# Optimization experiments

Measured on AMD Instinct MI355X. Metric: run time of the kernel, lower is better.

The kernel has to match this reference:

```python
import jax, jax.numpy as jnp
import numpy as np
from jax.ops import segment_sum, segment_max

N_NODES = 100000
N_EDGES = 1600000
F_DIM = 64
N_GRAPHS = 64
K_HOPS = 3
EPS = 1e-5


def setup_inputs() -> dict:
    key = jax.random.key(0)
    ks = jax.random.split(key, 8)
    x = jax.random.normal(ks[0], (N_NODES, F_DIM), dtype=jnp.float32)
    edge_index = jax.random.randint(ks[1], (2, N_EDGES), 0, N_NODES, dtype=jnp.int32)
    batch = jnp.sort(jax.random.randint(ks[2], (N_NODES,), 0, N_GRAPHS, dtype=jnp.int32))
    edge_weight = jax.random.uniform(ks[3], (N_EDGES,), dtype=jnp.float32)
    # TAGConv params: K+1 hop-wise linear weights (no per-lin bias) + one output bias
    W = jax.random.normal(ks[4], (K_HOPS + 1, F_DIM, F_DIM), dtype=jnp.float32) * 0.05
    b = jnp.zeros((F_DIM,), dtype=jnp.float32)
    # GraphNorm params
    gn_weight = jnp.ones((F_DIM,), dtype=jnp.float32)
    gn_bias = jnp.zeros((F_DIM,), dtype=jnp.float32)
    gn_mean_scale = jnp.ones((F_DIM,), dtype=jnp.float32)
    return {"x": x, "edge_index": edge_index, "batch": batch, "edge_weight": edge_weight,
            "W": W, "b": b, "gn_weight": gn_weight, "gn_bias": gn_bias,
            "gn_mean_scale": gn_mean_scale}


def reference(x, edge_index, batch, edge_weight, W, b, gn_weight, gn_bias, gn_mean_scale):
    src, dst = edge_index[0], edge_index[1]

    # --- TAGConv: gcn_norm without self-loops ---
    deg = segment_sum(edge_weight, dst, num_segments=N_NODES)            # [N]
    dis = jnp.where(deg > 0, jax.lax.rsqrt(deg), 0.0)                    # deg^{-1/2}, inf -> 0
    norm = dis[src] * edge_weight * dis[dst]                             # [E]

    # out = sum_k (A_norm^k x) W_k + b
    out = x @ W[0]
    h = x
    for k in range(1, K_HOPS + 1):
        h = segment_sum(norm[:, None] * h[src], dst, num_segments=N_NODES)  # [N, F]
        out = out + h @ W[k]
    out = out + b

    # --- GraphNorm: per-graph mean/var with learnable mean_scale ---
    cnt = segment_sum(jnp.ones((N_NODES,), out.dtype), batch, num_segments=N_GRAPHS)
    cnt = jnp.maximum(cnt, 1.0)[:, None]                                  # [G, 1]
    mean = segment_sum(out, batch, num_segments=N_GRAPHS) / cnt          # [G, F]
    centered = out - mean[batch] * gn_mean_scale                         # [N, F]
    var = segment_sum(centered * centered, batch, num_segments=N_GRAPHS) / cnt
    hn = gn_weight * centered / jnp.sqrt(var + EPS)[batch] + gn_bias

    # --- residual + ReLU (add_residue=True) ---
    h_emb = jax.nn.relu(hn + x)                                          # [N, F]

    # --- global mean + max pooling ---
    mean_pool = segment_sum(h_emb, batch, num_segments=N_GRAPHS) / cnt   # [G, F]
    max_pool = segment_max(h_emb, batch, num_segments=N_GRAPHS)          # [G, F]
    flat = jnp.concatenate([mean_pool, max_pool], axis=-1)               # [G, 2F]

    return (h_emb, flat)
```

## Files before the change

kernel.cpp:

```cpp
#include <hip/hip_runtime.h>
#include <hip/hip_bf16.h>

#define NN 100000
#define NE 1600000
#define NG 64
#define FD 64
#define EPSV 1e-5f

typedef __hip_bfloat16 bf16;
typedef __attribute__((ext_vector_type(8))) short bf16x8;
typedef __attribute__((ext_vector_type(4))) float f32x4;

__device__ __forceinline__ float ldb(bf16 v) { return __bfloat162float(v); }
__device__ __forceinline__ bf16 f2b(float v) { return __float2bfloat16(v); }
__device__ __forceinline__ float b2f_bits(short s) {
    return __uint_as_float(((unsigned)(unsigned short)s) << 16);
}

#define NB1 391
#define CB 625
#define EPB 2560
#define CCN (NB1 * CB)
#define SCB2 ((CCN + 2047) / 2048)

__device__ __forceinline__ int xcd_chunk(int bid, int nwg) {
    int q = nwg >> 3, r = nwg & 7;
    int xcd = bid & 7, j = bid >> 3;
    return (xcd < r ? xcd * (q + 1) : r * (q + 1) + (xcd - r) * q) + j;
}

constexpr size_t ALGN(size_t x) { return (x + 255) & ~(size_t)255; }
constexpr size_t OFF_GSUM = 0;
constexpr size_t OFF_GSSQ = OFF_GSUM + ALGN((size_t)NG * FD * 4);
constexpr size_t OFF_GCNT = OFF_GSSQ + ALGN((size_t)NG * FD * 4);
constexpr size_t OFF_PSUM = OFF_GCNT + ALGN((size_t)NG * 4);
constexpr size_t OFF_PMAX = OFF_PSUM + ALGN((size_t)NG * FD * 4);
constexpr size_t ZERO_BYTES = OFF_PMAX + ALGN((size_t)NG * FD * 4);
constexpr size_t OFF_CNT  = ZERO_BYTES;
constexpr size_t OFF_DIS  = OFF_CNT  + ALGN((size_t)NN * 4);
constexpr size_t OFF_ROWP = OFF_DIS  + ALGN((size_t)NN * 4);
constexpr size_t OFF_BSUM = OFF_ROWP + ALGN((size_t)NN * 4);
constexpr size_t OFF_WT   = OFF_BSUM + ALGN(256 * 4);
constexpr size_t OFF_CSR  = OFF_WT   + ALGN(16384 * 2);
constexpr size_t OFF_H    = OFF_CSR  + ALGN((size_t)NE * 8);
constexpr size_t OFF_OUT  = OFF_H    + ALGN((size_t)NN * 256 * 2);
constexpr size_t OFF_CSRT = OFF_OUT;
constexpr size_t OFF_CC   = OFF_CSRT + ALGN((size_t)NE * 8);
static_assert(OFF_CC + (size_t)CCN * 4 - OFF_OUT <= (size_t)NN * FD * 4, "alias overflow");

#define XCB 6250
__global__ __launch_bounds__(256) void coarse_fused_kernel(const int* __restrict__ dst,
                                                           int* __restrict__ cc,
                                                           const float* __restrict__ x,
                                                           bf16* __restrict__ H,
                                                           const float* __restrict__ W,
                                                           bf16* __restrict__ Wt) {
    int b = blockIdx.x;
    if (b < CB) {
        __shared__ int hist[NB1];
        for (int i = threadIdx.x; i < NB1; i += 256) hist[i] = 0;
        __syncthreads();
        int e0 = b * EPB + threadIdx.x;
        #pragma unroll
        for (int i = 0; i < EPB / 256; i++)
            atomicAdd(&hist[dst[e0 + i * 256] >> 8], 1);
        __syncthreads();
        for (int i = threadIdx.x; i < NB1; i += 256)
            cc[(size_t)i * CB + b] = hist[i];
    } else if (b < CB + XCB) {
        int i = (b - CB) * 256 + threadIdx.x;
        float4 xv = ((const float4*)x)[i];
        bf16 t0 = f2b(xv.x), t1 = f2b(xv.y), t2 = f2b(xv.z), t3 = f2b(xv.w);
        ushort4 o;
        o.x = *(unsigned short*)&t0; o.y = *(unsigned short*)&t1;
        o.z = *(unsigned short*)&t2; o.w = *(unsigned short*)&t3;
        ((ushort4*)H)[i] = o;
    } else {
        int i = (b - CB - XCB) * 256 + threadIdx.x;
        int n = i & 63, kk = i >> 6;
        Wt[n * 256 + kk] = f2b(W[kk * 64 + n]);
    }
}

#define SCAN_BLK 256
#define SCAN_ITEMS 8
__global__ __launch_bounds__(SCAN_BLK) void scan_blocks(int* __restrict__ data,
                                                        int* __restrict__ bsum, int n) {
    __shared__ int lds[SCAN_BLK];
    int t = threadIdx.x, b = blockIdx.x;
    int base = b * SCAN_BLK * SCAN_ITEMS + t * SCAN_ITEMS;
    int v[SCAN_ITEMS];
    int s = 0;
    #pragma unroll
    for (int i = 0; i < SCAN_ITEMS; i++) {
        int idx = base + i;
        v[i] = (idx < n) ? data[idx] : 0;
        s += v[i];
    }
    lds[t] = s;
    __syncthreads();
    for (int off = 1; off < SCAN_BLK; off <<= 1) {
        int x = (t >= off) ? lds[t - off] : 0;
        __syncthreads();
        lds[t] += x;
        __syncthreads();
    }
    int excl = lds[t] - s;
    if (t == SCAN_BLK - 1) bsum[b] = lds[t];
    int run = excl;
    #pragma unroll
    for (int i = 0; i < SCAN_ITEMS; i++) {
        int idx = base + i;
        if (idx < n) data[idx] = run;
        run += v[i];
    }
}

__global__ __launch_bounds__(256) void scatter2_kernel(const int* __restrict__ src,
                                                       const int* __restrict__ dst,
                                                       const float* __restrict__ ew,
                                                       const int* __restrict__ cc,
                                                       const int* __restrict__ bsum,
                                                       int2* __restrict__ csrt) {
    __shared__ int sc[512];
    __shared__ int bp[128];
    __shared__ int gdel[NB1];
    __shared__ int2 stage[EPB];
    __shared__ int sdel[EPB];
    int t = threadIdx.x;
    int L = xcd_chunk(blockIdx.x, CB);

    sc[t] = 0; sc[t + 256] = 0;
    if (t < 128) bp[t] = (t < SCB2) ? bsum[t] : 0;
    __syncthreads();

    int br[EPB / 256], px[EPB / 256], pw[EPB / 256];
    #pragma unroll
    for (int i = 0; i < EPB / 256; i++) {
        int e = L * EPB + i * 256 + t;
        int d = dst[e];
        int bk = d >> 8;
        int rk = atomicAdd(&sc[bk], 1);
        br[i] = bk | (rk << 9);
        px[i] = src[e] | ((d & 255) << 17);
        pw[i] = __float_as_int(ew[e]);
    }
    __syncthreads();

    for (int off = 1; off < 512; off <<= 1) {
        int a0 = (t >= off) ? sc[t - off] : 0;
        int a1 = sc[t + 256 - off];
        int a2 = (off < 128 && t < 128 && t >= off) ? bp[t - off] : 0;
        __syncthreads();
        sc[t] += a0; sc[t + 256] += a1;
        if (off < 128 && t < 128) bp[t] += a2;
        __syncthreads();
    }

    for (int i = t; i < NB1; i += 256) {
        int idx = i * CB + L;
        int k = idx >> 11;
        int gpref = (k > 0) ? bp[k - 1] : 0;
        gdel[i] = cc[idx] + gpref - ((i > 0) ? sc[i - 1] : 0);
    }
    __syncthreads();

    #pragma unroll
    for (int i = 0; i < EPB / 256; i++) {
        int bk = br[i] & 511;
        int rk = br[i] >> 9;
        int slot = ((bk > 0) ? sc[bk - 1] : 0) + rk;
        stage[slot] = make_int2(px[i], pw[i]);
        sdel[slot] = gdel[bk];
    }
    __syncthreads();

    for (int j = t; j < EPB; j += 256)
        csrt[(size_t)(sdel[j] + j)] = stage[j];
}

__global__ __launch_bounds__(256) void fine_kernel(const int* __restrict__ cc,
                                                   const int* __restrict__ bsum,
                                                   const int2* __restrict__ csrt,
                                                   int2* __restrict__ csr,
                                                   int* __restrict__ rowp,
                                                   int* __restrict__ cnts,
                                                   float* __restrict__ dis) {
    __shared__ int hist[256];
    __shared__ float degw[256];
    __shared__ int pref[256];
    __shared__ int fcur[256];
    __shared__ int bp[128];
    __shared__ int bounds[2];
    int b = blockIdx.x;
    int t = threadIdx.x;
    hist[t] = 0; degw[t] = 0.f;
    if (t < 128) bp[t] = (t < SCB2) ? bsum[t] : 0;
    __syncthreads();
    for (int off = 1; off < 128; off <<= 1) {
        int x = (t < 128 && t >= off) ? bp[t - off] : 0;
        __syncthreads();
        if (t < 128) bp[t] += x;
        __syncthreads();
    }
    if (t == 0) {
        int i0 = b * CB, k0 = i0 >> 11;
        bounds[0] = cc[i0] + ((k0 > 0) ? bp[k0 - 1] : 0);
        if (b == NB1 - 1) bounds[1] = NE;
        else {
            int i1 = (b + 1) * CB, k1 = i1 >> 11;
            bounds[1] = cc[i1] + ((k1 > 0) ? bp[k1 - 1] : 0);
        }
    }
    __syncthreads();
    int base = bounds[0];
    int cnt = bounds[1] - base;

    for (int j = t; j < cnt; j += 256) {
        int2 e = csrt[base + j];
        int f = e.x >> 17;
        atomicAdd(&hist[f], 1);
        atomicAdd(&degw[f], __int_as_float(e.y));
    }
    __syncthreads();
    int hv = hist[t];
    pref[t] = hv;
    __syncthreads();
    for (int off = 1; off < 256; off <<= 1) {
        int x = (t >= off) ? pref[t - off] : 0;
        __syncthreads();
        pref[t] += x;
        __syncthreads();
    }
    int ex = pref[t] - hv;
    fcur[t] = ex;
    int node = b * 256 + t;
    if (node < NN) {
        rowp[node] = base + ex;
        cnts[node] = hv;
        float s = degw[t];
        dis[node] = (s > 0.f) ? rsqrtf(s) : 0.f;
    }
    __syncthreads();
    for (int j = t; j < cnt; j += 256) {
        int2 e = csrt[base + j];
        int f = e.x >> 17;
        int pos = atomicAdd(&fcur[f], 1);
        csr[base + pos] = make_int2(e.x & 0x1FFFF, e.y);
    }
}

template <bool FIRST>
__device__ __forceinline__ void row_accum_gen(const bf16* __restrict__ hin,
                                              int2* cp, int cnt,
                                              const float* __restrict__ dis,
                                              int sub, int fl, float a[8]) {
    if (cnt <= 24) {
        int2 e0 = (sub < cnt) ? cp[sub] : make_int2(0, 0);
        int2 e1 = (8 + sub < cnt) ? cp[8 + sub] : make_int2(0, 0);
        int2 e2 = (16 + sub < cnt) ? cp[16 + sub] : make_int2(0, 0);
        bf16x8 v0 = *(const bf16x8*)(hin + (size_t)e0.x * 64 + fl * 8);
        bf16x8 v1 = *(const bf16x8*)(hin + (size_t)e1.x * 64 + fl * 8);
        bf16x8 v2 = *(const bf16x8*)(hin + (size_t)e2.x * 64 + fl * 8);
        float w0 = __int_as_float(e0.y);
        float w1 = __int_as_float(e1.y);
        float w2 = __int_as_float(e2.y);
        if (FIRST) {
            w0 *= dis[e0.x]; w1 *= dis[e1.x]; w2 *= dis[e2.x];
            if (fl == 0) {
                if (sub < cnt)      cp[sub].y      = __float_as_int(w0);
                if (8 + sub < cnt)  cp[8 + sub].y  = __float_as_int(w1);
                if (16 + sub < cnt) cp[16 + sub].y = __float_as_int(w2);
            }
        }
        #pragma unroll
        for (int i = 0; i < 8; i++)
            a[i] += w0 * b2f_bits(v0[i]) + w1 * b2f_bits(v1[i]) + w2 * b2f_bits(v2[i]);
    } else {
        float b[8] = {0, 0, 0, 0, 0, 0, 0, 0};
        int j = 0;
        for (; j + 16 <= cnt; j += 16) {
            int2 e0 = cp[j + sub];
            int2 e1 = cp[j + 8 + sub];
            bf16x8 v0 = *(const bf16x8*)(hin + (size_t)e0.x * 64 + fl * 8);
            bf16x8 v1 = *(const bf16x8*)(hin + (size_t)e1.x * 64 + fl * 8);
            float w0 = __int_as_float(e0.y);
            float w1 = __int_as_float(e1.y);
            if (FIRST) {
                w0 *= dis[e0.x]; w1 *= dis[e1.x];
                if (fl == 0) {
                    cp[j + sub].y     = __float_as_int(w0);
                    cp[j + 8 + sub].y = __float_as_int(w1);
                }
            }
            #pragma unroll
            for (int i = 0; i < 8; i++) a[i] += w0 * b2f_bits(v0[i]);
            #pragma unroll
            for (int i = 0; i < 8; i++) b[i] += w1 * b2f_bits(v1[i]);
        }
        for (; j < cnt; j += 8) {
            int jj = j + sub;
            int2 e = (jj < cnt) ? cp[jj] : make_int2(0, 0);
            bf16x8 v = *(const bf16x8*)(hin + (size_t)e.x * 64 + fl * 8);
            float w = __int_as_float(e.y);
            if (FIRST) {
                w *= dis[e.x];
                if (fl == 0 && jj < cnt) cp[jj].y = __float_as_int(w);
            }
            #pragma unroll
            for (int i = 0; i < 8; i++) a[i] += w * b2f_bits(v[i]);
        }
        #pragma unroll
        for (int i = 0; i < 8; i++) a[i] += b[i];
    }
}

template <bool FIRST>
__global__ __launch_bounds__(256) void hop_kernel(const bf16* __restrict__ hin,
                                                  bf16* __restrict__ hout,
                                                  const int* __restrict__ rowp,
                                                  const int* __restrict__ cnts,
                                                  int2* __restrict__ csr,
                                                  const float* __restrict__ dis) {
    int pair = blockIdx.x * 4 + (threadIdx.x >> 6);
    int rowA = pair * 2;
    if (rowA >= NN) return;
    rowA = __builtin_amdgcn_readfirstlane(rowA);
    int rowB = rowA + 1;
    int lane = threadIdx.x & 63;
    int sub = lane >> 3;
    int fl = lane & 7;

    int stA = rowp[rowA], cnA = cnts[rowA];
    int stB = rowp[rowB], cnB = cnts[rowB];
    float drA = dis[rowA], drB = dis[rowB];
    int2* cpA = csr + stA;
    int2* cpB = csr + stB;

    float a[8] = {0, 0, 0, 0, 0, 0, 0, 0};
    float c[8] = {0, 0, 0, 0, 0, 0, 0, 0};

    if (cnA <= 24 && cnB <= 24) {
        int2 eA0 = (sub < cnA) ? cpA[sub] : make_int2(0, 0);
        int2 eA1 = (8 + sub < cnA) ? cpA[8 + sub] : make_int2(0, 0);
        int2 eA2 = (16 + sub < cnA) ? cpA[16 + sub] : make_int2(0, 0);
        int2 eB0 = (sub < cnB) ? cpB[sub] : make_int2(0, 0);
        int2 eB1 = (8 + sub < cnB) ? cpB[8 + sub] : make_int2(0, 0);
        int2 eB2 = (16 + sub < cnB) ? cpB[16 + sub] : make_int2(0, 0);
        const bf16* hf = hin + fl * 8;
        bf16x8 vA0 = *(const bf16x8*)(hf + (size_t)eA0.x * 64);
        bf16x8 vA1 = *(const bf16x8*)(hf + (size_t)eA1.x * 64);
        bf16x8 vA2 = *(const bf16x8*)(hf + (size_t)eA2.x * 64);
        bf16x8 vB0 = *(const bf16x8*)(hf + (size_t)eB0.x * 64);
        bf16x8 vB1 = *(const bf16x8*)(hf + (size_t)eB1.x * 64);
        bf16x8 vB2 = *(const bf16x8*)(hf + (size_t)eB2.x * 64);
        float wA0 = __int_as_float(eA0.y);
        float wA1 = __int_as_float(eA1.y);
        float wA2 = __int_as_float(eA2.y);
        float wB0 = __int_as_float(eB0.y);
        float wB1 = __int_as_float(eB1.y);
        float wB2 = __int_as_float(eB2.y);
        if (FIRST) {
            wA0 *= dis[eA0.x]; wA1 *= dis[eA1.x]; wA2 *= dis[eA2.x];
            wB0 *= dis[eB0.x]; wB1 *= dis[eB1.x]; wB2 *= dis[eB2.x];
            if (fl == 0) {
                if (sub < cnA)      cpA[sub].y      = __float_as_int(wA0);
                if (8 + sub < cnA)  cpA[8 + sub].y  = __float_as_int(wA1);
                if (16 + sub < cnA) cpA[16 + sub].y = __float_as_int(wA2);
                if (sub < cnB)      cpB[sub].y      = __float_as_int(wB0);
                if (8 + sub < cnB)  cpB[8 + sub].y  = __float_as_int(wB1);
                if (16 + sub < cnB) cpB[16 + sub].y = __float_as_int(wB2);
            }
        }
        #pragma unroll
        for (int i = 0; i < 8; i++) {
            a[i] = wA0 * b2f_bits(vA0[i]) + wA1 * b2f_bits(vA1[i]) + wA2 * b2f_bits(vA2[i]);
            c[i] = wB0 * b2f_bits(vB0[i]) + wB1 * b2f_bits(vB1[i]) + wB2 * b2f_bits(vB2[i]);
        }
    } else {
        row_accum_gen<FIRST>(hin, cpA, cnA, dis, sub, fl, a);
        row_accum_gen<FIRST>(hin, cpB, cnB, dis, sub, fl, c);
    }

    #pragma unroll
    for (int i = 0; i < 8; i++) { a[i] += __shfl_xor(a[i], 8);  c[i] += __shfl_xor(c[i], 8); }
    #pragma unroll
    for (int i = 0; i < 8; i++) { a[i] += __shfl_xor(a[i], 16); c[i] += __shfl_xor(c[i], 16); }
    #pragma unroll
    for (int i = 0; i < 8; i++) { a[i] += __shfl_xor(a[i], 32); c[i] += __shfl_xor(c[i], 32); }

    if (sub == 0) {
        bf16x8 ovA, ovB;
        #pragma unroll
        for (int i = 0; i < 8; i++) {
            bf16 tA = f2b(a[i] * drA);
            bf16 tB = f2b(c[i] * drB);
            ovA[i] = *(short*)&tA;
            ovB[i] = *(short*)&tB;
        }
        *(bf16x8*)(hout + (size_t)rowA * 64 + fl * 8) = ovA;
        *(bf16x8*)(hout + (size_t)rowB * 64 + fl * 8) = ovB;
    }
}

#define GWAVES 1024
#define NT (NN / 16)

__global__ __launch_bounds__(256, 1) void gemm_kernel(const bf16* __restrict__ H,
                                                      const bf16* __restrict__ Wt,
                                                      const float* __restrict__ bias,
                                                      float* __restrict__ outb) {
    int wave = threadIdx.x >> 6;
    int lane = threadIdx.x & 63;
    int m = lane & 15, q = lane >> 4;
    int w = blockIdx.x * 4 + wave;

    bf16x8 B[4][8];
    #pragma unroll
    for (int n = 0; n < 4; n++) {
        const bf16* brow = Wt + (size_t)(n * 16 + m) * 256 + q * 8;
        #pragma unroll
        for (int ks = 0; ks < 8; ks++) B[n][ks] = *(const bf16x8*)(brow + ks * 32);
    }
    float bv[4];
    #pragma unroll
    for (int n = 0; n < 4; n++) bv[n] = bias[n * 16 + m];

    if (w >= NT) return;

    bf16x8 A0[8], A1[8];

    #define LOADA(dst_, t_)                                                      \
        {                                                                        \
            _Pragma("unroll")                                                    \
            for (int ks = 0; ks < 8; ks++)                                       \
                dst_[ks] = *(const bf16x8*)(H +                                  \
                    ((size_t)(ks >> 1) * NN + (size_t)((t_)*16 + m)) * 64 +      \
                    (ks & 1) * 32 + q * 8);                                      \
        }

    #define COMP(src_, t_)                                                   \
        {                                                                    \
            _Pragma("unroll")                                                \
            for (int n = 0; n < 4; n++) {                                    \
                f32x4 acc = {0.f, 0.f, 0.f, 0.f};                            \
                _Pragma("unroll")                                            \
                for (int ks = 0; ks < 8; ks++)                               \
                    acc = __builtin_amdgcn_mfma_f32_16x16x32_bf16(           \
                        src_[ks], B[n][ks], acc, 0, 0, 0);                   \
                _Pragma("unroll")                                            \
                for (int r = 0; r < 4; r++)                                  \
                    outb[(size_t)((t_)*16 + q * 4 + r) * 64 + n * 16 + m] =  \
                        acc[r] + bv[n];                                      \
            }                                                                \
        }

    int t = w;
    LOADA(A0, t)
    while (true) {
        int t1 = t + GWAVES;
        if (t1 < NT) LOADA(A1, t1)
        COMP(A0, t)
        if (t1 >= NT) return;
        int t2 = t1 + GWAVES;
        if (t2 < NT) LOADA(A0, t2)
        COMP(A1, t1)
        if (t2 >= NT) return;
        t = t2;
    }
    #undef LOADA
    #undef COMP
}

#define CH 32
#define STAT_WAVES ((NN + CH - 1) / CH)
#define STAT_BLOCKS ((STAT_WAVES * 64 + 255) / 256)

__global__ __launch_bounds__(256) void stats_kernel(const float* __restrict__ outb,
                                                    const int* __restrict__ batch,
                                                    float* __restrict__ gsum,
                                                    float* __restrict__ gssq,
                                                    float* __restrict__ gcnt) {
    int wid = (blockIdx.x * 256 + threadIdx.x) >> 6;
    int lane = threadIdx.x & 63;
    int n0 = wid * CH;
    if (n0 >= NN) return;
    int n1 = min(n0 + CH, NN);
    int g0 = batch[n0];
    if (n1 == n0 + CH && batch[n1 - 1] == g0) {
        float s = 0.f, s2 = 0.f;
        #pragma unroll
        for (int i = 0; i < CH; i++) {
            float v = outb[(size_t)(n0 + i) * 64 + lane];
            s += v; s2 += v * v;
        }
        atomicAdd(&gsum[g0 * 64 + lane], s);
        atomicAdd(&gssq[g0 * 64 + lane], s2);
        if (lane == 0) atomicAdd(&gcnt[g0], (float)CH);
    } else {
        int cur = g0; float s = 0.f, s2 = 0.f; int cl = 0;
        for (int i = n0; i < n1; i++) {
            int g = batch[i];
            if (g != cur) {
                atomicAdd(&gsum[cur * 64 + lane], s);
                atomicAdd(&gssq[cur * 64 + lane], s2);
                if (lane == 0) atomicAdd(&gcnt[cur], (float)cl);
                s = 0.f; s2 = 0.f; cl = 0; cur = g;
            }
            float v = outb[(size_t)i * 64 + lane];
            s += v; s2 += v * v; cl++;
        }
        atomicAdd(&gsum[cur * 64 + lane], s);
        atomicAdd(&gssq[cur * 64 + lane], s2);
        if (lane == 0) atomicAdd(&gcnt[cur], (float)cl);
    }
}

__device__ __forceinline__ void graph_mr(const float* gsum, const float* gssq,
                                         const float* gcnt, int g, int lane, float ms,
                                         float& mm, float& r) {
    float c = fmaxf(gcnt[g], 1.f);
    float mean = gsum[g * 64 + lane] / c;
    float msq = gssq[g * 64 + lane] / c;
    mm = mean * ms;
    float var = fmaxf(msq - 2.f * mm * mean + mm * mm, 0.f);
    r = rsqrtf(var + EPSV);
}

__global__ __launch_bounds__(256) void final_kernel(const float* __restrict__ outb,
                                                    const int* __restrict__ batch,
                                                    const float* __restrict__ xg,
                                                    const float* __restrict__ gsum,
                                                    const float* __restrict__ gssq,
                                                    const float* __restrict__ gcnt,
                                                    const float* __restrict__ gw_,
                                                    const float* __restrict__ gb_,
                                                    const float* __restrict__ ms_,
                                                    float* __restrict__ psum,
                                                    int* __restrict__ pmax,
                                                    float* __restrict__ hemb) {
    int wid = (blockIdx.x * 256 + threadIdx.x) >> 6;
    int lane = threadIdx.x & 63;
    int n0 = wid * CH;
    if (n0 >= NN) return;
    int n1 = min(n0 + CH, NN);
    float gw = gw_[lane], gb = gb_[lane], ms = ms_[lane];
    int g0 = batch[n0];
    if (n1 == n0 + CH && batch[n1 - 1] == g0) {
        float m, r;
        graph_mr(gsum, gssq, gcnt, g0, lane, ms, m, r);
        float ps = 0.f, pm = 0.f;
        #pragma unroll
        for (int i = 0; i < CH; i++) {
            size_t idx = (size_t)(n0 + i) * 64 + lane;
            float hn = gw * (outb[idx] - m) * r + gb;
            float he = hn + xg[idx];
            he = he > 0.f ? he : 0.f;
            hemb[idx] = he;
            ps += he;
            pm = fmaxf(pm, he);
        }
        atomicAdd(&psum[g0 * 64 + lane], ps);
        atomicMax(&pmax[g0 * 64 + lane], __float_as_int(pm));
    } else {
        int cur = g0;
        float m, r;
        graph_mr(gsum, gssq, gcnt, cur, lane, ms, m, r);
        float ps = 0.f, pm = 0.f;
        for (int i = n0; i < n1; i++) {
            int g = batch[i];
            if (g != cur) {
                atomicAdd(&psum[cur * 64 + lane], ps);
                atomicMax(&pmax[cur * 64 + lane], __float_as_int(pm));
                ps = 0.f; pm = 0.f; cur = g;
                graph_mr(gsum, gssq, gcnt, cur, lane, ms, m, r);
            }
            size_t idx = (size_t)i * 64 + lane;
            float hn = gw * (outb[idx] - m) * r + gb;
            float he = hn + xg[idx];
            he = he > 0.f ? he : 0.f;
            hemb[idx] = he;
            ps += he;
            pm = fmaxf(pm, he);
        }
        atomicAdd(&psum[cur * 64 + lane], ps);
        atomicMax(&pmax[cur * 64 + lane], __float_as_int(pm));
    }
}

__global__ __launch_bounds__(256) void pool_kernel(const float* __restrict__ psum,
                                                   const int* __restrict__ pmax,
                                                   const float* __restrict__ gcnt,
                                                   float* __restrict__ flat) {
    int i = blockIdx.x * 256 + threadIdx.x;
    if (i >= NG * FD) return;
    int g = i >> 6, f = i & 63;
    float c = fmaxf(gcnt[g], 1.f);
    flat[(size_t)g * 128 + f] = psum[i] / c;
    flat[(size_t)g * 128 + 64 + f] = __int_as_float(pmax[i]);
}

extern "C" void kernel_launch(void* const* d_in, const int* in_sizes, int n_in,
                              void* d_out, int out_size, void* d_ws, size_t ws_size,
                              hipStream_t stream) {
    const float* x = (const float*)d_in[0];
    const int* ei = (const int*)d_in[1];
    const int* batch = (const int*)d_in[2];
    const float* ew = (const float*)d_in[3];
    const float* W = (const float*)d_in[4];
    const float* bias = (const float*)d_in[5];
    const float* gnw = (const float*)d_in[6];
    const float* gnb = (const float*)d_in[7];
    const float* gms = (const float*)d_in[8];

    const int* src = ei;
    const int* dst = ei + NE;

    char* ws = (char*)d_ws;
    float* gsum = (float*)(ws + OFF_GSUM);
    float* gssq = (float*)(ws + OFF_GSSQ);
    float* gcnt = (float*)(ws + OFF_GCNT);
    float* psum = (float*)(ws + OFF_PSUM);
    int* pmax = (int*)(ws + OFF_PMAX);
    int* cnts = (int*)(ws + OFF_CNT);
    float* dis = (float*)(ws + OFF_DIS);
    int* rowp = (int*)(ws + OFF_ROWP);
    int* bsum = (int*)(ws + OFF_BSUM);
    bf16* Wt = (bf16*)(ws + OFF_WT);
    int2* csr = (int2*)(ws + OFF_CSR);
    bf16* H = (bf16*)(ws + OFF_H);
    float* outb = (float*)(ws + OFF_OUT);
    int2* csrt = (int2*)(ws + OFF_CSRT);
    int* cc = (int*)(ws + OFF_CC);

    float* hemb = (float*)d_out;
    float* flat = hemb + (size_t)NN * FD;

    hipMemsetAsync(d_ws, 0, ZERO_BYTES, stream);

    const size_t PL = (size_t)NN * 64;
    const int HOPB = (NN / 2 + 3) / 4;
    const int GFB = (NG * FD + 255) / 256;

    coarse_fused_kernel<<<CB + XCB + 64, 256, 0, stream>>>(dst, cc, x, H, W, Wt);
    scan_blocks<<<SCB2, 256, 0, stream>>>(cc, bsum, CCN);
    scatter2_kernel<<<CB, 256, 0, stream>>>(src, dst, ew, cc, bsum, csrt);
    fine_kernel<<<NB1, 256, 0, stream>>>(cc, bsum, csrt, csr, rowp, cnts, dis);

    hop_kernel<true><<<HOPB, 256, 0, stream>>>(H, H + PL, rowp, cnts, csr, dis);
    hop_kernel<false><<<HOPB, 256, 0, stream>>>(H + PL, H + 2 * PL, rowp, cnts, csr, dis);
    hop_kernel<false><<<HOPB, 256, 0, stream>>>(H + 2 * PL, H + 3 * PL, rowp, cnts, csr, dis);

    gemm_kernel<<<GWAVES / 4, 256, 0, stream>>>(H, Wt, bias, outb);

    stats_kernel<<<STAT_BLOCKS, 256, 0, stream>>>(outb, batch, gsum, gssq, gcnt);
    final_kernel<<<STAT_BLOCKS, 256, 0, stream>>>(outb, batch, x, gsum, gssq, gcnt,
                                                  gnw, gnb, gms, psum, pmax, hemb);
    pool_kernel<<<GFB, 256, 0, stream>>>(psum, pmax, gcnt, flat);
}
```

Before: 326.7 us.

## Fuse third propagation hop into the output GEMM via shared memory

The third hop's aggregation is computed per 16-row tile inside a new fused kernel. Its results go to LDS and feed directly into the MFMA GEMM instead of being written to and re-read from global memory. This removes one kernel launch and the global round-trip of the hop-3 features. In exchange, half the waves sit idle during the GEMM, the weights are reloaded per block, and the persistent, software-pipelined GEMM loop is gone.

```diff
diff --git a/kernel.cpp b/kernel.cpp
--- a/kernel.cpp
+++ b/kernel.cpp
@@ -316,29 +316,21 @@
 }
 
 template <bool FIRST>
-__global__ __launch_bounds__(256) void hop_kernel(const bf16* __restrict__ hin,
-                                                  bf16* __restrict__ hout,
-                                                  const int* __restrict__ rowp,
-                                                  const int* __restrict__ cnts,
-                                                  int2* __restrict__ csr,
-                                                  const float* __restrict__ dis) {
-    int pair = blockIdx.x * 4 + (threadIdx.x >> 6);
-    int rowA = pair * 2;
-    if (rowA >= NN) return;
-    rowA = __builtin_amdgcn_readfirstlane(rowA);
-    int rowB = rowA + 1;
-    int lane = threadIdx.x & 63;
-    int sub = lane >> 3;
-    int fl = lane & 7;
-
+__device__ __forceinline__ void hop_pair_body(const bf16* __restrict__ hin,
+                                              int rowA, int rowB,
+                                              const int* __restrict__ rowp,
+                                              const int* __restrict__ cnts,
+                                              int2* __restrict__ csr,
+                                              const float* __restrict__ dis,
+                                              int sub, int fl,
+                                              float a[8], float c[8]) {
     int stA = rowp[rowA], cnA = cnts[rowA];
     int stB = rowp[rowB], cnB = cnts[rowB];
-    float drA = dis[rowA], drB = dis[rowB];
     int2* cpA = csr + stA;
     int2* cpB = csr + stB;
 
-    float a[8] = {0, 0, 0, 0, 0, 0, 0, 0};
-    float c[8] = {0, 0, 0, 0, 0, 0, 0, 0};
+    #pragma unroll
+    for (int i = 0; i < 8; i++) { a[i] = 0.f; c[i] = 0.f; }
 
     if (cnA <= 24 && cnB <= 24) {
         int2 eA0 = (sub < cnA) ? cpA[sub] : make_int2(0, 0);
@@ -388,6 +380,27 @@
     for (int i = 0; i < 8; i++) { a[i] += __shfl_xor(a[i], 16); c[i] += __shfl_xor(c[i], 16); }
     #pragma unroll
     for (int i = 0; i < 8; i++) { a[i] += __shfl_xor(a[i], 32); c[i] += __shfl_xor(c[i], 32); }
+}
+
+template <bool FIRST>
+__global__ __launch_bounds__(256) void hop_kernel(const bf16* __restrict__ hin,
+                                                  bf16* __restrict__ hout,
+                                                  const int* __restrict__ rowp,
+                                                  const int* __restrict__ cnts,
+                                                  int2* __restrict__ csr,
+                                                  const float* __restrict__ dis) {
+    int pair = blockIdx.x * 4 + (threadIdx.x >> 6);
+    int rowA = pair * 2;
+    if (rowA >= NN) return;
+    rowA = __builtin_amdgcn_readfirstlane(rowA);
+    int rowB = rowA + 1;
+    int lane = threadIdx.x & 63;
+    int sub = lane >> 3;
+    int fl = lane & 7;
+
+    float drA = dis[rowA], drB = dis[rowB];
+    float a[8], c[8];
+    hop_pair_body<FIRST>(hin, rowA, rowB, rowp, cnts, csr, dis, sub, fl, a, c);
 
     if (sub == 0) {
         bf16x8 ovA, ovB;
@@ -403,73 +416,69 @@
     }
 }
 
-#define GWAVES 1024
 #define NT (NN / 16)
 
-__global__ __launch_bounds__(256, 1) void gemm_kernel(const bf16* __restrict__ H,
-                                                      const bf16* __restrict__ Wt,
-                                                      const float* __restrict__ bias,
-                                                      float* __restrict__ outb) {
+__global__ __launch_bounds__(512) void hop3_gemm_kernel(const bf16* __restrict__ hin,
+                                                        const bf16* __restrict__ H,
+                                                        const bf16* __restrict__ Wt,
+                                                        const float* __restrict__ bias,
+                                                        const int* __restrict__ rowp,
+                                                        const int* __restrict__ cnts,
+                                                        int2* __restrict__ csr,
+                                                        const float* __restrict__ dis,
+                                                        float* __restrict__ outb) {
+    __shared__ bf16 sh3[16][72];
     int wave = threadIdx.x >> 6;
     int lane = threadIdx.x & 63;
+    int row0 = blockIdx.x * 16;
+
+    {
+        int rowA = row0 + wave * 2;
+        rowA = __builtin_amdgcn_readfirstlane(rowA);
+        int rowB = rowA + 1;
+        int sub = lane >> 3, fl = lane & 7;
+        float drA = dis[rowA], drB = dis[rowB];
+        float a[8], c[8];
+        hop_pair_body<false>(hin, rowA, rowB, rowp, cnts, csr, dis, sub, fl, a, c);
+        if (sub == 0) {
+            bf16x8 ovA, ovB;
+            #pragma unroll
+            for (int i = 0; i < 8; i++) {
+                bf16 tA = f2b(a[i] * drA);
+                bf16 tB = f2b(c[i] * drB);
+                ovA[i] = *(short*)&tA;
+                ovB[i] = *(short*)&tB;
+            }
+            *(bf16x8*)(&sh3[wave * 2 + 0][fl * 8]) = ovA;
+            *(bf16x8*)(&sh3[wave * 2 + 1][fl * 8]) = ovB;
+        }
+    }
+    __syncthreads();
+    if (wave >= 4) return;
+
     int m = lane & 15, q = lane >> 4;
-    int w = blockIdx.x * 4 + wave;
-
-    bf16x8 B[4][8];
-    #pragma unroll
-    for (int n = 0; n < 4; n++) {
-        const bf16* brow = Wt + (size_t)(n * 16 + m) * 256 + q * 8;
-        #pragma unroll
-        for (int ks = 0; ks < 8; ks++) B[n][ks] = *(const bf16x8*)(brow + ks * 32);
-    }
-    float bv[4];
-    #pragma unroll
-    for (int n = 0; n < 4; n++) bv[n] = bias[n * 16 + m];
-
-    if (w >= NT) return;
-
-    bf16x8 A0[8], A1[8];
-
-    #define LOADA(dst_, t_)                                                      \
-        {                                                                        \
-            _Pragma("unroll")                                                    \
-            for (int ks = 0; ks < 8; ks++)                                       \
-                dst_[ks] = *(const bf16x8*)(H +                                  \
-                    ((size_t)(ks >> 1) * NN + (size_t)((t_)*16 + m)) * 64 +      \
-                    (ks & 1) * 32 + q * 8);                                      \
-        }
-
-    #define COMP(src_, t_)                                                   \
-        {                                                                    \
-            _Pragma("unroll")                                                \
-            for (int n = 0; n < 4; n++) {                                    \
-                f32x4 acc = {0.f, 0.f, 0.f, 0.f};                            \
-                _Pragma("unroll")                                            \
-                for (int ks = 0; ks < 8; ks++)                               \
-                    acc = __builtin_amdgcn_mfma_f32_16x16x32_bf16(           \
-                        src_[ks], B[n][ks], acc, 0, 0, 0);                   \
-                _Pragma("unroll")                                            \
-                for (int r = 0; r < 4; r++)                                  \
-                    outb[(size_t)((t_)*16 + q * 4 + r) * 64 + n * 16 + m] =  \
-                        acc[r] + bv[n];                                      \
-            }                                                                \
-        }
-
-    int t = w;
-    LOADA(A0, t)
-    while (true) {
-        int t1 = t + GWAVES;
-        if (t1 < NT) LOADA(A1, t1)
-        COMP(A0, t)
-        if (t1 >= NT) return;
-        int t2 = t1 + GWAVES;
-        if (t2 < NT) LOADA(A0, t2)
-        COMP(A1, t1)
-        if (t2 >= NT) return;
-        t = t2;
-    }
-    #undef LOADA
-    #undef COMP
+    int c0 = wave * 16;
+    bf16x8 B[8];
+    const bf16* brow = Wt + (size_t)(c0 + m) * 256 + q * 8;
+    #pragma unroll
+    for (int ks = 0; ks < 8; ks++) B[ks] = *(const bf16x8*)(brow + ks * 32);
+    bf16x8 A[8];
+    #pragma unroll
+    for (int ks = 0; ks < 6; ks++)
+        A[ks] = *(const bf16x8*)(H + ((size_t)(ks >> 1) * NN + (size_t)(row0 + m)) * 64 +
+                                 (ks & 1) * 32 + q * 8);
+    A[6] = *(const bf16x8*)(&sh3[m][q * 8]);
+    A[7] = *(const bf16x8*)(&sh3[m][32 + q * 8]);
+
+    f32x4 acc = {0.f, 0.f, 0.f, 0.f};
+    #pragma unroll
+    for (int ks = 0; ks < 8; ks++)
+        acc = __builtin_amdgcn_mfma_f32_16x16x32_bf16(A[ks], B[ks], acc, 0, 0, 0);
+
+    float bv = bias[c0 + m];
+    #pragma unroll
+    for (int r = 0; r < 4; r++)
+        outb[(size_t)(row0 + q * 4 + r) * 64 + c0 + m] = acc[r] + bv;
 }
 
 #define CH 32
@@ -649,9 +658,8 @@
 
     hop_kernel<true><<<HOPB, 256, 0, stream>>>(H, H + PL, rowp, cnts, csr, dis);
     hop_kernel<false><<<HOPB, 256, 0, stream>>>(H + PL, H + 2 * PL, rowp, cnts, csr, dis);
-    hop_kernel<false><<<HOPB, 256, 0, stream>>>(H + 2 * PL, H + 3 * PL, rowp, cnts, csr, dis);
-
-    gemm_kernel<<<GWAVES / 4, 256, 0, stream>>>(H, Wt, bias, outb);
+    hop3_gemm_kernel<<<NT, 512, 0, stream>>>(H + 2 * PL, H, Wt, bias,
+                                             rowp, cnts, csr, dis, outb);
 
     stats_kernel<<<STAT_BLOCKS, 256, 0, stream>>>(outb, batch, gsum, gssq, gcnt);
     final_kernel<<<STAT_BLOCKS, 256, 0, stream>>>(outb, batch, x, gsum, gssq, gcnt,
```

Measured after the change: 352.7 us. 8.0% more time.
